# Kernel optimization log

Measured on AMD Instinct MI355X. Metric: run time of the kernel, lower is better.

The kernel has to match this reference:

```python
import jax, jax.numpy as jnp
import numpy as np

EMB = 512       # emb_dim
H = 8           # n_heads
HD = EMB // H   # head_dim = 64
FREQ = 64       # freq_features
PERIOD = 0.1
N = 2048


def setup_inputs() -> dict:
    key = jax.random.key(0)
    ks = jax.random.split(key, 6)
    x = jax.random.normal(ks[0], (1, N, EMB), dtype=jnp.float32)
    v = jax.random.normal(ks[1], (1, N, 3), dtype=jnp.float32)
    vec_map = v / jnp.linalg.norm(v, axis=-1, keepdims=True)  # unit direction vectors
    s_in = 1.0 / np.sqrt(EMB)
    W_qkv = jax.random.normal(ks[2], (EMB, 3 * EMB), dtype=jnp.float32) * s_in
    b_qkv = jnp.zeros((3 * EMB,), dtype=jnp.float32)
    W_bias = jax.random.normal(ks[3], (FREQ, H), dtype=jnp.float32) * (1.0 / np.sqrt(FREQ))
    b_bias = jnp.zeros((H,), dtype=jnp.float32)
    W_out = jax.random.normal(ks[4], (EMB, EMB), dtype=jnp.float32) * s_in
    b_out = jnp.zeros((EMB,), dtype=jnp.float32)
    return {"x": x, "vec_map": vec_map, "W_qkv": W_qkv, "b_qkv": b_qkv,
            "W_bias": W_bias, "b_bias": b_bias, "W_out": W_out, "b_out": b_out}


def reference(x, vec_map, W_qkv, b_qkv, W_bias, b_bias, W_out, b_out):
    batch_dim = x.shape[:-2]
    n = x.shape[-2]
    # QKV projection -> (*, N, H, 3, HD)
    qkv = (x @ W_qkv + b_qkv).reshape(*batch_dim, n, H, 3, HD)
    q, k, v = (qkv[..., 0, :], qkv[..., 1, :], qkv[..., 2, :])
    # attention scores (*, Q, K, H), softmax over the K axis (axis=-2)
    attn = jnp.einsum('...qht,...kht->...qkh', q, k) / np.sqrt(HD)
    attn = jax.nn.softmax(attn, axis=-2)
    # relative bias from pairwise angles between direction vectors
    dot = jnp.einsum('...nc,...mc->...nm', vec_map, vec_map)
    angle = jnp.arccos(jnp.clip(dot, 0.0, 1.0)) / 0.001
    freqs = jnp.linspace(0.0, 1.0, FREQ // 2, dtype=jnp.float32) / PERIOD
    phase = freqs * angle[..., None]                      # (*, N, N, FREQ/2)
    pos = jnp.concatenate((jnp.sin(phase), jnp.cos(phase)), axis=-1)  # (*, N, N, FREQ)
    bias = pos @ W_bias + b_bias                          # (*, N, N, H)
    attn = attn + bias
    # weighted sum of values -> (*, N, EMB)
    y = jnp.einsum('...qkh,...kht->...qht', attn, v).reshape(*batch_dim, n, EMB)
    return y @ W_out + b_out
```

## Files before the change

kernel.cpp:

```cpp
#include <hip/hip_runtime.h>
#include <hip/hip_bf16.h>
#include <math.h>

#define NT 2048
#define EMBD 512
#define NH 8
#define QKV_LD 1536

typedef unsigned short u16;
typedef __attribute__((ext_vector_type(8))) short short8;
typedef __attribute__((ext_vector_type(4))) float v4f;

static __device__ __forceinline__ float bf2f(unsigned int u) {
    union { unsigned int i; float f; } c; c.i = u << 16; return c.f;
}
static __device__ __forceinline__ void unpack8(uint4 r, float* f) {
    f[0] = bf2f(r.x & 0xffffu); f[1] = bf2f(r.x >> 16);
    f[2] = bf2f(r.y & 0xffffu); f[3] = bf2f(r.y >> 16);
    f[4] = bf2f(r.z & 0xffffu); f[5] = bf2f(r.z >> 16);
    f[6] = bf2f(r.w & 0xffffu); f[7] = bf2f(r.w >> 16);
}
static __device__ __forceinline__ void unpack4(uint2 r, float* f) {
    f[0] = bf2f(r.x & 0xffffu); f[1] = bf2f(r.x >> 16);
    f[2] = bf2f(r.y & 0xffffu); f[3] = bf2f(r.y >> 16);
}
static __device__ __forceinline__ unsigned int f2bf(float x) {
    union { float f; unsigned int u; } c; c.f = x;
    return (c.u + 0x7fffu + ((c.u >> 16) & 1u)) >> 16;
}

__global__ __launch_bounds__(256) void split_x(const float* __restrict__ x,
    u16* __restrict__ xh, u16* __restrict__ xl)
{
    int i = (blockIdx.x * 256 + threadIdx.x) << 2;
    float4 v = *(const float4*)(x + i);
    float f[4] = {v.x, v.y, v.z, v.w};
    unsigned int hi[4], lo[4];
#pragma unroll
    for (int j = 0; j < 4; ++j) {
        hi[j] = f2bf(f[j]);
        lo[j] = f2bf(f[j] - bf2f(hi[j]));
    }
    uint2 wh; wh.x = hi[0] | (hi[1] << 16); wh.y = hi[2] | (hi[3] << 16);
    uint2 wl; wl.x = lo[0] | (lo[1] << 16); wl.y = lo[2] | (lo[3] << 16);
    *(uint2*)(xh + i) = wh;
    *(uint2*)(xl + i) = wl;
}

__global__ __launch_bounds__(256) void split_wt(const float* __restrict__ W,
    u16* __restrict__ wth, u16* __restrict__ wtl)
{
    __shared__ float tile[64][65];
    const int n0 = blockIdx.x << 6, k0 = blockIdx.y << 6;
    const int t = threadIdx.x;
    const int r = t >> 2, c4 = (t & 3) << 4;
#pragma unroll
    for (int j = 0; j < 4; ++j)
        *(float4*)&tile[r][c4 + (j << 2)] =
            *(const float4*)(W + (size_t)(k0 + r) * QKV_LD + n0 + c4 + (j << 2));
    __syncthreads();
    const int n_l = t >> 2;
    u16 th[16], tl[16];
#pragma unroll
    for (int j = 0; j < 16; ++j) {
        float f = tile[c4 + j][n_l];
        unsigned int h = f2bf(f);
        th[j] = (u16)h;
        tl[j] = (u16)f2bf(f - bf2f(h));
    }
    u16* dh = wth + (size_t)(n0 + n_l) * EMBD + k0 + c4;
    u16* dl = wtl + (size_t)(n0 + n_l) * EMBD + k0 + c4;
    *(uint4*)dh       = *(uint4*)&th[0];
    *(uint4*)(dh + 8) = *(uint4*)&th[8];
    *(uint4*)dl       = *(uint4*)&tl[0];
    *(uint4*)(dl + 8) = *(uint4*)&tl[8];
}

__global__ __launch_bounds__(256) void split_wout(const float* __restrict__ W,
    u16* __restrict__ wh, u16* __restrict__ wl)
{
    __shared__ float tile[64][65];
    const int n0 = blockIdx.x << 6, k0 = blockIdx.y << 6;
    const int t = threadIdx.x;
    const int r = t >> 2, c4 = (t & 3) << 4;
#pragma unroll
    for (int j = 0; j < 4; ++j)
        *(float4*)&tile[r][c4 + (j << 2)] =
            *(const float4*)(W + (size_t)(k0 + r) * EMBD + n0 + c4 + (j << 2));
    __syncthreads();
    const int n_l = t >> 2;
    u16 th[16], tl[16];
#pragma unroll
    for (int j = 0; j < 16; ++j) {
        float f = tile[c4 + j][n_l];
        unsigned int h = f2bf(f);
        th[j] = (u16)h;
        tl[j] = (u16)f2bf(f - bf2f(h));
    }
    u16* dh = wh + (size_t)(n0 + n_l) * EMBD + k0 + c4;
    u16* dl = wl + (size_t)(n0 + n_l) * EMBD + k0 + c4;
    *(uint4*)dh       = *(uint4*)&th[0];
    *(uint4*)(dh + 8) = *(uint4*)&th[8];
    *(uint4*)dl       = *(uint4*)&tl[0];
    *(uint4*)(dl + 8) = *(uint4*)&tl[8];
}

__global__ __launch_bounds__(256) void gemm_qkv_mfma(const u16* __restrict__ xh,
    const u16* __restrict__ xl, const u16* __restrict__ wth,
    const u16* __restrict__ wtl, const float* __restrict__ bias,
    u16* __restrict__ qkvb)
{
    const int n0 = blockIdx.x << 6, m0 = blockIdx.y << 6;
    const int w = threadIdx.x >> 6, lane = threadIdx.x & 63;
    const int wm = w >> 1, wn = w & 1;
    const int fr = lane & 15, kd = (lane >> 4) << 3;

    const u16* ah0 = xh + (size_t)(m0 + wm * 32 + fr) * EMBD + kd;
    const u16* al0 = xl + (size_t)(m0 + wm * 32 + fr) * EMBD + kd;
    const u16* bh0 = wth + (size_t)(n0 + wn * 32 + fr) * EMBD + kd;
    const u16* bl0 = wtl + (size_t)(n0 + wn * 32 + fr) * EMBD + kd;

    v4f acc[2][2] = {};
    for (int kc = 0; kc < EMBD; kc += 32) {
        short8 a_h[2], a_l[2], b_h[2], b_l[2];
#pragma unroll
        for (int im = 0; im < 2; ++im) {
            a_h[im] = *(const short8*)(ah0 + (size_t)im * 16 * EMBD + kc);
            a_l[im] = *(const short8*)(al0 + (size_t)im * 16 * EMBD + kc);
        }
#pragma unroll
        for (int in = 0; in < 2; ++in) {
            b_h[in] = *(const short8*)(bh0 + (size_t)in * 16 * EMBD + kc);
            b_l[in] = *(const short8*)(bl0 + (size_t)in * 16 * EMBD + kc);
        }
#pragma unroll
        for (int im = 0; im < 2; ++im)
#pragma unroll
            for (int in = 0; in < 2; ++in) {
                acc[im][in] = __builtin_amdgcn_mfma_f32_16x16x32_bf16(a_h[im], b_h[in], acc[im][in], 0, 0, 0);
                acc[im][in] = __builtin_amdgcn_mfma_f32_16x16x32_bf16(a_h[im], b_l[in], acc[im][in], 0, 0, 0);
                acc[im][in] = __builtin_amdgcn_mfma_f32_16x16x32_bf16(a_l[im], b_h[in], acc[im][in], 0, 0, 0);
            }
    }
    const int qr = (lane >> 4) << 2;
#pragma unroll
    for (int im = 0; im < 2; ++im)
#pragma unroll
        for (int in = 0; in < 2; ++in) {
            int n = n0 + wn * 32 + in * 16 + fr;
            float bv = bias[n];
#pragma unroll
            for (int r = 0; r < 4; ++r) {
                int m = m0 + wm * 32 + im * 16 + qr + r;
                qkvb[(size_t)m * QKV_LD + n] = (u16)f2bf(acc[im][in][r] + bv);
            }
        }
}

__global__ __launch_bounds__(256) void transpose_v(const u16* __restrict__ qkvb,
                                                   u16* __restrict__ Vt)
{
    __shared__ u16 tile[64][72];
    const int h = blockIdx.y, k0 = blockIdx.x << 6;
    const int t = threadIdx.x;
    {
        int r = t >> 2, cg = (t & 3) << 4;
        const u16* src = qkvb + (size_t)(k0 + r) * QKV_LD + h * 192 + 128 + cg;
        *(uint4*)&tile[r][cg]     = *(const uint4*)src;
        *(uint4*)&tile[r][cg + 8] = *(const uint4*)(src + 8);
    }
    __syncthreads();
    {
        int c = t >> 2, kg = (t & 3) << 4;
        u16 tmp[16];
#pragma unroll
        for (int j = 0; j < 16; ++j) tmp[j] = tile[kg + j][c];
        u16* dst = Vt + ((size_t)h * 64 + c) * NT + k0 + kg;
        *(uint4*)dst       = *(uint4*)&tmp[0];
        *(uint4*)(dst + 8) = *(uint4*)&tmp[8];
    }
}

__global__ __launch_bounds__(256) void scores_mfma(const u16* __restrict__ qkvb,
                                                   u16* __restrict__ s,
                                                   float* __restrict__ zbuf)
{
    const int h = blockIdx.z;
    const int k0 = blockIdx.x << 7;
    const int q0 = (blockIdx.y << 7) + ((threadIdx.x >> 6) << 5);
    const int lane = threadIdx.x & 63;
    const int fr = lane & 15;
    const int kd = (lane >> 4) << 3;

    const u16* qbase = qkvb + (size_t)(q0 + fr) * QKV_LD + h * 192 + kd;
    const u16* kbase = qkvb + (size_t)(k0 + fr) * QKV_LD + h * 192 + 64 + kd;

    short8 aq[2][2];
    aq[0][0] = *(const short8*)(qbase);
    aq[0][1] = *(const short8*)(qbase + 32);
    aq[1][0] = *(const short8*)(qbase + (size_t)16 * QKV_LD);
    aq[1][1] = *(const short8*)(qbase + (size_t)16 * QKV_LD + 32);

    v4f acc[2][8] = {};
#pragma unroll
    for (int nt = 0; nt < 8; ++nt) {
        short8 b0 = *(const short8*)(kbase + (size_t)nt * 16 * QKV_LD);
        short8 b1 = *(const short8*)(kbase + (size_t)nt * 16 * QKV_LD + 32);
        acc[0][nt] = __builtin_amdgcn_mfma_f32_16x16x32_bf16(aq[0][0], b0, acc[0][nt], 0, 0, 0);
        acc[0][nt] = __builtin_amdgcn_mfma_f32_16x16x32_bf16(aq[0][1], b1, acc[0][nt], 0, 0, 0);
        acc[1][nt] = __builtin_amdgcn_mfma_f32_16x16x32_bf16(aq[1][0], b0, acc[1][nt], 0, 0, 0);
        acc[1][nt] = __builtin_amdgcn_mfma_f32_16x16x32_bf16(aq[1][1], b1, acc[1][nt], 0, 0, 0);
    }
    const int qr = (lane >> 4) << 2;
#pragma unroll
    for (int i = 0; i < 2; ++i)
#pragma unroll
        for (int nt = 0; nt < 8; ++nt)
#pragma unroll
            for (int r = 0; r < 4; ++r) {
                int q = q0 + (i << 4) + qr + r;
                int k = k0 + (nt << 4) + fr;
                s[((size_t)h * NT + q) * NT + k] = (u16)f2bf(acc[i][nt][r] * 0.125f);
            }
    float es[2][4];
#pragma unroll
    for (int i = 0; i < 2; ++i)
#pragma unroll
        for (int r = 0; r < 4; ++r) {
            float sum = 0.f;
#pragma unroll
            for (int nt = 0; nt < 8; ++nt)
                sum += __expf(acc[i][nt][r] * 0.125f);
            es[i][r] = sum;
        }
#pragma unroll
    for (int off = 1; off < 16; off <<= 1)
#pragma unroll
        for (int i = 0; i < 2; ++i)
#pragma unroll
            for (int r = 0; r < 4; ++r)
                es[i][r] += __shfl_xor(es[i][r], off);
    if (fr == 0) {
#pragma unroll
        for (int i = 0; i < 2; ++i)
#pragma unroll
            for (int r = 0; r < 4; ++r)
                atomicAdd(zbuf + h * NT + q0 + (i << 4) + qr + r, es[i][r]);
    }
}

__global__ __launch_bounds__(256) void bias_kernel(u16* __restrict__ s,
    const float* __restrict__ vec, const float* __restrict__ Wb,
    const float* __restrict__ bb, const float* __restrict__ zbuf)
{
    __shared__ float flds[32];
    __shared__ float vql[96], vkl[96];
    __shared__ float bbl[8];
    __shared__ float ang_lds[1025];
    __shared__ float biasl[8 * 1057];
    __shared__ float clipb[8];
    __shared__ unsigned char flagl[1024];
    __shared__ u16 list[1040];
    __shared__ int cnt;

    const int t = threadIdx.x;
    int b = blockIdx.x, tq = 0, rem = 64;
    while (b >= rem) { b -= rem; ++tq; --rem; }
    const int tk = tq + b;
    const int q0 = tq << 5, k0 = tk << 5;

    if (t == 0) cnt = 0;
    if (t < 32) flds[t] = __fdiv_rn(__fdiv_rn((float)t, 31.0f), 0.1f);
    else if (t < 128) vql[t - 32] = vec[q0 * 3 + (t - 32)];
    else if (t < 224) vkl[t - 128] = vec[k0 * 3 + (t - 128)];
    else if (t < 232) bbl[t - 224] = bb[t - 224];
    __syncthreads();

    {
        const int qq = t & 31, kb = (t >> 5) << 2;
        const int lane = t & 63;
        const float a0 = vql[qq * 3], a1 = vql[qq * 3 + 1], a2 = vql[qq * 3 + 2];
#pragma unroll
        for (int j = 0; j < 4; ++j) {
            const int kk = kb + j;
            const int p = (qq << 5) + kk;
            float c0 = vkl[kk * 3], c1 = vkl[kk * 3 + 1], c2 = vkl[kk * 3 + 2];
            float dot = __fadd_rn(__fadd_rn(__fmul_rn(a0, c0), __fmul_rn(a1, c1)),
                                  __fmul_rn(a2, c2));
            float dotc = fminf(fmaxf(dot, 0.0f), 1.0f);
            ang_lds[p] = __fdiv_rn(acosf(dotc), 0.001f);
            int live = (dot > 0.0f) ? 1 : 0;
            flagl[p] = (unsigned char)(1 - live);
            unsigned long long m = __ballot(live);
            int base = 0;
            if (lane == 0) base = atomicAdd(&cnt, __popcll(m));
            base = __shfl(base, 0);
            if (live)
                list[base + __popcll(m & ((1ull << lane) - 1ull))] = (u16)p;
        }
    }
    __syncthreads();
    if (t == 0) {
        int c = cnt;
        int padded = (c + 15) & ~15;
        for (int i = c; i < padded; ++i) list[i] = 1024;
        float zero = fabsf(vql[0]) * 0.0f;
        float zc = fminf(fmaxf(zero, 0.0f), 1.0f);
        ang_lds[1024] = __fdiv_rn(acosf(zc), 0.001f);
        cnt = padded;
    }
    __syncthreads();
    const int ntiles = cnt >> 4;

    {
        const int w = t >> 6, lane = t & 63;
        const int fr = lane & 15, kd = (lane >> 4) << 3, qr = (lane >> 4) << 2;
        short8 BS, BC;
#pragma unroll
        for (int j = 0; j < 8; ++j) {
            float ws = (fr < 8) ? Wb[(kd + j) * 8 + fr] : 0.0f;
            float wc = (fr < 8) ? Wb[(32 + kd + j) * 8 + fr] : 0.0f;
            BS[j] = (short)f2bf(ws);
            BC[j] = (short)f2bf(wc);
        }
        if (w == 0) {
            float ang = ang_lds[1024];
            short8 AS, AC;
#pragma unroll
            for (int j = 0; j < 8; ++j) {
                float ph = __fmul_rn(flds[kd + j], ang);
                float rv = ph * 0.15915494309189535f;
                float rf = rv - floorf(rv);
                AS[j] = (short)f2bf(__builtin_amdgcn_sinf(rf));
                AC[j] = (short)f2bf(__builtin_amdgcn_cosf(rf));
            }
            v4f c = {};
            c = __builtin_amdgcn_mfma_f32_16x16x32_bf16(AS, BS, c, 0, 0, 0);
            c = __builtin_amdgcn_mfma_f32_16x16x32_bf16(AC, BC, c, 0, 0, 0);
            if (fr < 8) clipb[fr] = c[0];
        }
        for (int i = w; i < ntiles; i += 4) {
            float ang = ang_lds[list[(i << 4) + fr]];
            short8 AS, AC;
#pragma unroll
            for (int j = 0; j < 8; ++j) {
                float ph = __fmul_rn(flds[kd + j], ang);
                float rv = ph * 0.15915494309189535f;
                float rf = rv - floorf(rv);
                AS[j] = (short)f2bf(__builtin_amdgcn_sinf(rf));
                AC[j] = (short)f2bf(__builtin_amdgcn_cosf(rf));
            }
            v4f c = {};
            c = __builtin_amdgcn_mfma_f32_16x16x32_bf16(AS, BS, c, 0, 0, 0);
            c = __builtin_amdgcn_mfma_f32_16x16x32_bf16(AC, BC, c, 0, 0, 0);
            if (fr < 8) {
#pragma unroll
                for (int r = 0; r < 4; ++r) {
                    int p = list[(i << 4) + qr + r];
                    if (p < 1024)
                        biasl[fr * 1057 + (p >> 5) * 33 + (p & 31)] = c[r];
                }
            }
        }
    }
    __syncthreads();

    const int r = t >> 3;
    const int cg = (t & 7) << 2;
    {
        const int q = q0 + r;
#pragma unroll
        for (int h = 0; h < 8; ++h) {
            const float iz = 1.0f / zbuf[h * NT + q];
            const float bv = bbl[h];
            const size_t base = ((size_t)h * NT + q) * NT + k0 + cg;
            uint2 raw = *(const uint2*)(s + base);
            float v[4]; unpack4(raw, v);
            unsigned int o[4];
#pragma unroll
            for (int j = 0; j < 4; ++j) {
                int p = (r << 5) + cg + j;
                float bias = flagl[p] ? clipb[h] : biasl[h * 1057 + r * 33 + cg + j];
                o[j] = f2bf(__expf(v[j]) * iz + bias + bv);
            }
            uint2 wv; wv.x = o[0] | (o[1] << 16); wv.y = o[2] | (o[3] << 16);
            *(uint2*)(s + base) = wv;
        }
    }
    if (tk != tq) {
        const int q = k0 + r;
#pragma unroll
        for (int h = 0; h < 8; ++h) {
            const float iz = 1.0f / zbuf[h * NT + q];
            const float bv = bbl[h];
            const size_t base = ((size_t)h * NT + q) * NT + q0 + cg;
            uint2 raw = *(const uint2*)(s + base);
            float v[4]; unpack4(raw, v);
            unsigned int o[4];
#pragma unroll
            for (int j = 0; j < 4; ++j) {
                int p = ((cg + j) << 5) + r;
                float bias = flagl[p] ? clipb[h] : biasl[h * 1057 + (cg + j) * 33 + r];
                o[j] = f2bf(__expf(v[j]) * iz + bias + bv);
            }
            uint2 wv; wv.x = o[0] | (o[1] << 16); wv.y = o[2] | (o[3] << 16);
            *(uint2*)(s + base) = wv;
        }
    }
}

__global__ __launch_bounds__(256) void attnv_mfma(const u16* __restrict__ attn,
    const u16* __restrict__ Vt, float* __restrict__ ypart)
{
    const int h = blockIdx.y, z = blockIdx.z;
    const int q0 = (blockIdx.x << 6) + ((threadIdx.x >> 6) << 4);
    const int lane = threadIdx.x & 63;
    const int fr = lane & 15;
    const int kd = (lane >> 4) << 3;
    const int kbase = z << 9;

    const u16* arow  = attn + (size_t)(h * NT + q0 + fr) * NT + kbase + kd;
    const u16* vbase = Vt + ((size_t)h * 64 + fr) * NT + kbase + kd;

    v4f c[4] = {};
    for (int ks = 0; ks < 512; ks += 32) {
        short8 a = *(const short8*)(arow + ks);
#pragma unroll
        for (int nt = 0; nt < 4; ++nt) {
            short8 bv = *(const short8*)(vbase + (size_t)nt * 16 * NT + ks);
            c[nt] = __builtin_amdgcn_mfma_f32_16x16x32_bf16(a, bv, c[nt], 0, 0, 0);
        }
    }
    float* yp = ypart + (size_t)z * NT * EMBD;
    const int qr = (lane >> 4) << 2;
#pragma unroll
    for (int nt = 0; nt < 4; ++nt)
#pragma unroll
        for (int r = 0; r < 4; ++r)
            yp[(size_t)(q0 + qr + r) * EMBD + (h << 6) + (nt << 4) + fr] = c[nt][r];
}

__global__ __launch_bounds__(256) void reduce_y(const float* __restrict__ parts,
    u16* __restrict__ yh, u16* __restrict__ yl)
{
    const int MN = NT * EMBD;
    int i = (blockIdx.x * 256 + threadIdx.x) << 2;
    float4 acc = *(const float4*)(parts + i);
#pragma unroll
    for (int sp = 1; sp < 4; ++sp) {
        float4 p = *(const float4*)(parts + (size_t)sp * MN + i);
        acc.x += p.x; acc.y += p.y; acc.z += p.z; acc.w += p.w;
    }
    float f[4] = {acc.x, acc.y, acc.z, acc.w};
    unsigned int hi[4], lo[4];
#pragma unroll
    for (int j = 0; j < 4; ++j) {
        hi[j] = f2bf(f[j]);
        lo[j] = f2bf(f[j] - bf2f(hi[j]));
    }
    uint2 wh; wh.x = hi[0] | (hi[1] << 16); wh.y = hi[2] | (hi[3] << 16);
    uint2 wl; wl.x = lo[0] | (lo[1] << 16); wl.y = lo[2] | (lo[3] << 16);
    *(uint2*)(yh + i) = wh;
    *(uint2*)(yl + i) = wl;
}

__global__ __launch_bounds__(256) void gemm_out_mfma(const u16* __restrict__ yh,
    const u16* __restrict__ yl, const u16* __restrict__ wh,
    const u16* __restrict__ wl, const float* __restrict__ bias,
    float* __restrict__ out)
{
    const int n0 = blockIdx.x << 6, m0 = blockIdx.y << 6;
    const int w = threadIdx.x >> 6, lane = threadIdx.x & 63;
    const int wm = w >> 1, wn = w & 1;
    const int fr = lane & 15, kd = (lane >> 4) << 3;

    const u16* ah0 = yh + (size_t)(m0 + wm * 32 + fr) * EMBD + kd;
    const u16* al0 = yl + (size_t)(m0 + wm * 32 + fr) * EMBD + kd;
    const u16* bh0 = wh + (size_t)(n0 + wn * 32 + fr) * EMBD + kd;
    const u16* bl0 = wl + (size_t)(n0 + wn * 32 + fr) * EMBD + kd;

    v4f acc[2][2] = {};
    for (int kc = 0; kc < EMBD; kc += 32) {
        short8 a_h[2], a_l[2], b_h[2], b_l[2];
#pragma unroll
        for (int im = 0; im < 2; ++im) {
            a_h[im] = *(const short8*)(ah0 + (size_t)im * 16 * EMBD + kc);
            a_l[im] = *(const short8*)(al0 + (size_t)im * 16 * EMBD + kc);
        }
#pragma unroll
        for (int in = 0; in < 2; ++in) {
            b_h[in] = *(const short8*)(bh0 + (size_t)in * 16 * EMBD + kc);
            b_l[in] = *(const short8*)(bl0 + (size_t)in * 16 * EMBD + kc);
        }
#pragma unroll
        for (int im = 0; im < 2; ++im)
#pragma unroll
            for (int in = 0; in < 2; ++in) {
                acc[im][in] = __builtin_amdgcn_mfma_f32_16x16x32_bf16(a_h[im], b_h[in], acc[im][in], 0, 0, 0);
                acc[im][in] = __builtin_amdgcn_mfma_f32_16x16x32_bf16(a_h[im], b_l[in], acc[im][in], 0, 0, 0);
                acc[im][in] = __builtin_amdgcn_mfma_f32_16x16x32_bf16(a_l[im], b_h[in], acc[im][in], 0, 0, 0);
            }
    }
    const int qr = (lane >> 4) << 2;
#pragma unroll
    for (int im = 0; im < 2; ++im)
#pragma unroll
        for (int in = 0; in < 2; ++in) {
            int n = n0 + wn * 32 + in * 16 + fr;
            float bv = bias[n];
#pragma unroll
            for (int r = 0; r < 4; ++r) {
                int m = m0 + wm * 32 + im * 16 + qr + r;
                out[(size_t)m * EMBD + n] = acc[im][in][r] + bv;
            }
        }
}

extern "C" void kernel_launch(void* const* d_in, const int* in_sizes, int n_in,
                              void* d_out, int out_size, void* d_ws, size_t ws_size,
                              hipStream_t stream)
{
    const float* x    = (const float*)d_in[0];
    const float* vec  = (const float*)d_in[1];
    const float* Wqkv = (const float*)d_in[2];
    const float* bqkv = (const float*)d_in[3];
    const float* Wb   = (const float*)d_in[4];
    const float* bb   = (const float*)d_in[5];
    const float* Wout = (const float*)d_in[6];
    const float* bout = (const float*)d_in[7];
    float* out = (float*)d_out;

    char* ws = (char*)d_ws;
    u16*   qkvb  = (u16*)(ws);
    u16*   sbuf  = (u16*)(ws + 6291456);
    u16*   Vt    = (u16*)(ws + 73400320);
    float* zbuf  = (float*)(ws + 75497472);
    u16*   yh    = (u16*)(ws + 75628544);
    u16*   yl    = (u16*)(ws + 77725696);
    float* parts = (float*)(ws + 79822848);
    u16*   xh    = (u16*)(ws + 79822848);
    u16*   xl    = (u16*)(ws + 81920000);
    u16*   wth   = (u16*)(ws + 84017152);
    u16*   wtl   = (u16*)(ws + 85590016);
    u16*   woth  = (u16*)(ws + 79822848);
    u16*   wotl  = (u16*)(ws + 80347136);

    hipMemsetAsync(zbuf, 0, NH * NT * sizeof(float), stream);
    split_x<<<1024, 256, 0, stream>>>(x, xh, xl);
    split_wt<<<dim3(24, 8), 256, 0, stream>>>(Wqkv, wth, wtl);
    gemm_qkv_mfma<<<dim3(24, 32), 256, 0, stream>>>(xh, xl, wth, wtl, bqkv, qkvb);
    transpose_v<<<dim3(32, 8), 256, 0, stream>>>(qkvb, Vt);
    scores_mfma<<<dim3(16, 16, 8), 256, 0, stream>>>(qkvb, sbuf, zbuf);
    bias_kernel<<<2080, 256, 0, stream>>>(sbuf, vec, Wb, bb, zbuf);
    attnv_mfma<<<dim3(32, 8, 4), 256, 0, stream>>>(sbuf, Vt, parts);
    reduce_y<<<1024, 256, 0, stream>>>(parts, yh, yl);
    split_wout<<<dim3(8, 8), 256, 0, stream>>>(Wout, woth, wotl);
    gemm_out_mfma<<<dim3(8, 32), 256, 0, stream>>>(yh, yl, woth, wotl, bout, out);
}
```

Baseline: 278.2 us.

## Stage score tiles in LDS for coalesced stores; drop bias compaction list

The scores kernel now writes its bf16 score tile to shared memory first, then stores it to global memory as coalesced 16-byte rows instead of scattered 2-byte writes. The bias kernel removes the ballot/atomic compaction of positive-dot pairs and the clipped-bias special case, and computes the sin/cos MFMA bias for all 1024 pairs in every tile. This cuts uncoalesced stores and branching, but adds redundant trig work on pairs whose angle is clipped. split_wout is merged into split_wt through a leading-dimension parameter.

```diff
diff --git a/kernel.cpp b/kernel.cpp
--- a/kernel.cpp
+++ b/kernel.cpp
@@ -14,12 +14,6 @@
 static __device__ __forceinline__ float bf2f(unsigned int u) {
     union { unsigned int i; float f; } c; c.i = u << 16; return c.f;
 }
-static __device__ __forceinline__ void unpack8(uint4 r, float* f) {
-    f[0] = bf2f(r.x & 0xffffu); f[1] = bf2f(r.x >> 16);
-    f[2] = bf2f(r.y & 0xffffu); f[3] = bf2f(r.y >> 16);
-    f[4] = bf2f(r.z & 0xffffu); f[5] = bf2f(r.z >> 16);
-    f[6] = bf2f(r.w & 0xffffu); f[7] = bf2f(r.w >> 16);
-}
 static __device__ __forceinline__ void unpack4(uint2 r, float* f) {
     f[0] = bf2f(r.x & 0xffffu); f[1] = bf2f(r.x >> 16);
     f[2] = bf2f(r.y & 0xffffu); f[3] = bf2f(r.y >> 16);
@@ -48,7 +42,7 @@
 }
 
 __global__ __launch_bounds__(256) void split_wt(const float* __restrict__ W,
-    u16* __restrict__ wth, u16* __restrict__ wtl)
+    u16* __restrict__ wth, u16* __restrict__ wtl, int ld)
 {
     __shared__ float tile[64][65];
     const int n0 = blockIdx.x << 6, k0 = blockIdx.y << 6;
@@ -57,7 +51,7 @@
 #pragma unroll
     for (int j = 0; j < 4; ++j)
         *(float4*)&tile[r][c4 + (j << 2)] =
-            *(const float4*)(W + (size_t)(k0 + r) * QKV_LD + n0 + c4 + (j << 2));
+            *(const float4*)(W + (size_t)(k0 + r) * ld + n0 + c4 + (j << 2));
     __syncthreads();
     const int n_l = t >> 2;
     u16 th[16], tl[16];
@@ -70,35 +64,6 @@
     }
     u16* dh = wth + (size_t)(n0 + n_l) * EMBD + k0 + c4;
     u16* dl = wtl + (size_t)(n0 + n_l) * EMBD + k0 + c4;
-    *(uint4*)dh       = *(uint4*)&th[0];
-    *(uint4*)(dh + 8) = *(uint4*)&th[8];
-    *(uint4*)dl       = *(uint4*)&tl[0];
-    *(uint4*)(dl + 8) = *(uint4*)&tl[8];
-}
-
-__global__ __launch_bounds__(256) void split_wout(const float* __restrict__ W,
-    u16* __restrict__ wh, u16* __restrict__ wl)
-{
-    __shared__ float tile[64][65];
-    const int n0 = blockIdx.x << 6, k0 = blockIdx.y << 6;
-    const int t = threadIdx.x;
-    const int r = t >> 2, c4 = (t & 3) << 4;
-#pragma unroll
-    for (int j = 0; j < 4; ++j)
-        *(float4*)&tile[r][c4 + (j << 2)] =
-            *(const float4*)(W + (size_t)(k0 + r) * EMBD + n0 + c4 + (j << 2));
-    __syncthreads();
-    const int n_l = t >> 2;
-    u16 th[16], tl[16];
-#pragma unroll
-    for (int j = 0; j < 16; ++j) {
-        float f = tile[c4 + j][n_l];
-        unsigned int h = f2bf(f);
-        th[j] = (u16)h;
-        tl[j] = (u16)f2bf(f - bf2f(h));
-    }
-    u16* dh = wh + (size_t)(n0 + n_l) * EMBD + k0 + c4;
-    u16* dl = wl + (size_t)(n0 + n_l) * EMBD + k0 + c4;
     *(uint4*)dh       = *(uint4*)&th[0];
     *(uint4*)(dh + 8) = *(uint4*)&th[8];
     *(uint4*)dl       = *(uint4*)&tl[0];
@@ -185,15 +150,18 @@
                                                    u16* __restrict__ s,
                                                    float* __restrict__ zbuf)
 {
+    __shared__ u16 tile[128][144];
     const int h = blockIdx.z;
-    const int k0 = blockIdx.x << 7;
-    const int q0 = (blockIdx.y << 7) + ((threadIdx.x >> 6) << 5);
+    const int kb = blockIdx.x << 7;
+    const int qb = blockIdx.y << 7;
+    const int w = threadIdx.x >> 6;
+    const int q0 = qb + (w << 5);
     const int lane = threadIdx.x & 63;
     const int fr = lane & 15;
     const int kd = (lane >> 4) << 3;
 
     const u16* qbase = qkvb + (size_t)(q0 + fr) * QKV_LD + h * 192 + kd;
-    const u16* kbase = qkvb + (size_t)(k0 + fr) * QKV_LD + h * 192 + 64 + kd;
+    const u16* kbase = qkvb + (size_t)(kb + fr) * QKV_LD + h * 192 + 64 + kd;
 
     short8 aq[2][2];
     aq[0][0] = *(const short8*)(qbase);
@@ -217,11 +185,9 @@
 #pragma unroll
         for (int nt = 0; nt < 8; ++nt)
 #pragma unroll
-            for (int r = 0; r < 4; ++r) {
-                int q = q0 + (i << 4) + qr + r;
-                int k = k0 + (nt << 4) + fr;
-                s[((size_t)h * NT + q) * NT + k] = (u16)f2bf(acc[i][nt][r] * 0.125f);
-            }
+            for (int r = 0; r < 4; ++r)
+                tile[(w << 5) + (i << 4) + qr + r][(nt << 4) + fr] =
+                    (u16)f2bf(acc[i][nt][r] * 0.125f);
     float es[2][4];
 #pragma unroll
     for (int i = 0; i < 2; ++i)
@@ -247,6 +213,15 @@
             for (int r = 0; r < 4; ++r)
                 atomicAdd(zbuf + h * NT + q0 + (i << 4) + qr + r, es[i][r]);
     }
+    __syncthreads();
+    const int row0 = threadIdx.x >> 4;
+    const int col = (threadIdx.x & 15) << 3;
+#pragma unroll
+    for (int l = 0; l < 8; ++l) {
+        int row = row0 + (l << 4);
+        *(uint4*)(s + ((size_t)h * NT + qb + row) * NT + kb + col) =
+            *(uint4*)&tile[row][col];
+    }
 }
 
 __global__ __launch_bounds__(256) void bias_kernel(u16* __restrict__ s,
@@ -256,12 +231,8 @@
     __shared__ float flds[32];
     __shared__ float vql[96], vkl[96];
     __shared__ float bbl[8];
-    __shared__ float ang_lds[1025];
+    __shared__ float ang_lds[1057];
     __shared__ float biasl[8 * 1057];
-    __shared__ float clipb[8];
-    __shared__ unsigned char flagl[1024];
-    __shared__ u16 list[1040];
-    __shared__ int cnt;
 
     const int t = threadIdx.x;
     int b = blockIdx.x, tq = 0, rem = 64;
@@ -269,7 +240,6 @@
     const int tk = tq + b;
     const int q0 = tq << 5, k0 = tk << 5;
 
-    if (t == 0) cnt = 0;
     if (t < 32) flds[t] = __fdiv_rn(__fdiv_rn((float)t, 31.0f), 0.1f);
     else if (t < 128) vql[t - 32] = vec[q0 * 3 + (t - 32)];
     else if (t < 224) vkl[t - 128] = vec[k0 * 3 + (t - 128)];
@@ -278,39 +248,18 @@
 
     {
         const int qq = t & 31, kb = (t >> 5) << 2;
-        const int lane = t & 63;
         const float a0 = vql[qq * 3], a1 = vql[qq * 3 + 1], a2 = vql[qq * 3 + 2];
 #pragma unroll
         for (int j = 0; j < 4; ++j) {
             const int kk = kb + j;
-            const int p = (qq << 5) + kk;
             float c0 = vkl[kk * 3], c1 = vkl[kk * 3 + 1], c2 = vkl[kk * 3 + 2];
             float dot = __fadd_rn(__fadd_rn(__fmul_rn(a0, c0), __fmul_rn(a1, c1)),
                                   __fmul_rn(a2, c2));
             float dotc = fminf(fmaxf(dot, 0.0f), 1.0f);
-            ang_lds[p] = __fdiv_rn(acosf(dotc), 0.001f);
-            int live = (dot > 0.0f) ? 1 : 0;
-            flagl[p] = (unsigned char)(1 - live);
-            unsigned long long m = __ballot(live);
-            int base = 0;
-            if (lane == 0) base = atomicAdd(&cnt, __popcll(m));
-            base = __shfl(base, 0);
-            if (live)
-                list[base + __popcll(m & ((1ull << lane) - 1ull))] = (u16)p;
-        }
-    }
-    __syncthreads();
-    if (t == 0) {
-        int c = cnt;
-        int padded = (c + 15) & ~15;
-        for (int i = c; i < padded; ++i) list[i] = 1024;
-        float zero = fabsf(vql[0]) * 0.0f;
-        float zc = fminf(fmaxf(zero, 0.0f), 1.0f);
-        ang_lds[1024] = __fdiv_rn(acosf(zc), 0.001f);
-        cnt = padded;
-    }
-    __syncthreads();
-    const int ntiles = cnt >> 4;
+            ang_lds[qq * 33 + kk] = __fdiv_rn(acosf(dotc), 0.001f);
+        }
+    }
+    __syncthreads();
 
     {
         const int w = t >> 6, lane = t & 63;
@@ -323,8 +272,9 @@
             BS[j] = (short)f2bf(ws);
             BC[j] = (short)f2bf(wc);
         }
-        if (w == 0) {
-            float ang = ang_lds[1024];
+        for (int tt = w; tt < 64; tt += 4) {
+            int p = (tt << 4) + fr;
+            float ang = ang_lds[(p >> 5) * 33 + (p & 31)];
             short8 AS, AC;
 #pragma unroll
             for (int j = 0; j < 8; ++j) {
@@ -337,28 +287,11 @@
             v4f c = {};
             c = __builtin_amdgcn_mfma_f32_16x16x32_bf16(AS, BS, c, 0, 0, 0);
             c = __builtin_amdgcn_mfma_f32_16x16x32_bf16(AC, BC, c, 0, 0, 0);
-            if (fr < 8) clipb[fr] = c[0];
-        }
-        for (int i = w; i < ntiles; i += 4) {
-            float ang = ang_lds[list[(i << 4) + fr]];
-            short8 AS, AC;
-#pragma unroll
-            for (int j = 0; j < 8; ++j) {
-                float ph = __fmul_rn(flds[kd + j], ang);
-                float rv = ph * 0.15915494309189535f;
-                float rf = rv - floorf(rv);
-                AS[j] = (short)f2bf(__builtin_amdgcn_sinf(rf));
-                AC[j] = (short)f2bf(__builtin_amdgcn_cosf(rf));
-            }
-            v4f c = {};
-            c = __builtin_amdgcn_mfma_f32_16x16x32_bf16(AS, BS, c, 0, 0, 0);
-            c = __builtin_amdgcn_mfma_f32_16x16x32_bf16(AC, BC, c, 0, 0, 0);
             if (fr < 8) {
 #pragma unroll
                 for (int r = 0; r < 4; ++r) {
-                    int p = list[(i << 4) + qr + r];
-                    if (p < 1024)
-                        biasl[fr * 1057 + (p >> 5) * 33 + (p & 31)] = c[r];
+                    int pp = (tt << 4) + qr + r;
+                    biasl[fr * 1057 + (pp >> 5) * 33 + (pp & 31)] = c[r];
                 }
             }
         }
@@ -379,8 +312,7 @@
             unsigned int o[4];
 #pragma unroll
             for (int j = 0; j < 4; ++j) {
-                int p = (r << 5) + cg + j;
-                float bias = flagl[p] ? clipb[h] : biasl[h * 1057 + r * 33 + cg + j];
+                float bias = biasl[h * 1057 + r * 33 + cg + j];
                 o[j] = f2bf(__expf(v[j]) * iz + bias + bv);
             }
             uint2 wv; wv.x = o[0] | (o[1] << 16); wv.y = o[2] | (o[3] << 16);
@@ -399,8 +331,7 @@
             unsigned int o[4];
 #pragma unroll
             for (int j = 0; j < 4; ++j) {
-                int p = ((cg + j) << 5) + r;
-                float bias = flagl[p] ? clipb[h] : biasl[h * 1057 + (cg + j) * 33 + r];
+                float bias = biasl[h * 1057 + (cg + j) * 33 + r];
                 o[j] = f2bf(__expf(v[j]) * iz + bias + bv);
             }
             uint2 wv; wv.x = o[0] | (o[1] << 16); wv.y = o[2] | (o[3] << 16);
@@ -547,13 +478,13 @@
 
     hipMemsetAsync(zbuf, 0, NH * NT * sizeof(float), stream);
     split_x<<<1024, 256, 0, stream>>>(x, xh, xl);
-    split_wt<<<dim3(24, 8), 256, 0, stream>>>(Wqkv, wth, wtl);
+    split_wt<<<dim3(24, 8), 256, 0, stream>>>(Wqkv, wth, wtl, QKV_LD);
     gemm_qkv_mfma<<<dim3(24, 32), 256, 0, stream>>>(xh, xl, wth, wtl, bqkv, qkvb);
     transpose_v<<<dim3(32, 8), 256, 0, stream>>>(qkvb, Vt);
     scores_mfma<<<dim3(16, 16, 8), 256, 0, stream>>>(qkvb, sbuf, zbuf);
     bias_kernel<<<2080, 256, 0, stream>>>(sbuf, vec, Wb, bb, zbuf);
     attnv_mfma<<<dim3(32, 8, 4), 256, 0, stream>>>(sbuf, Vt, parts);
     reduce_y<<<1024, 256, 0, stream>>>(parts, yh, yl);
-    split_wout<<<dim3(8, 8), 256, 0, stream>>>(Wout, woth, wotl);
+    split_wt<<<dim3(8, 8), 256, 0, stream>>>(Wout, woth, wotl, EMBD);
     gemm_out_mfma<<<dim3(8, 32), 256, 0, stream>>>(yh, yl, woth, wotl, bout, out);
 }
```

After: 274.6 us. Within noise of the previous version (-1.3%).
